# Kernel optimization log

Hardware: AMD Instinct MI355X
Metric: run time of the kernel (lower is better)

## Reference

```python
import jax, jax.numpy as jnp
import numpy as np

N_NODES = 50000
N_EDGES = 1600000
IN_FEAT = 128
OUT_FEAT = 128
NUM_RELS = 40


def setup_inputs() -> dict:
    key = jax.random.key(0)
    ks = jax.random.split(key, 8)
    h = jax.random.normal(ks[0], (N_NODES, IN_FEAT), dtype=jnp.float32)
    # Linear(in_feat, out_feat, bias=False): weight shape [out, in]
    W = jax.random.normal(ks[1], (OUT_FEAT, IN_FEAT), dtype=jnp.float32) / np.sqrt(IN_FEAT)
    # attn_fc: Linear(2*out_feat, 1, bias=False): weight shape [1, 2*out]
    attn_w = jax.random.normal(ks[2], (1, 2 * OUT_FEAT), dtype=jnp.float32) / np.sqrt(2 * OUT_FEAT)
    # Embedding(num_rels, 1, padding_idx=0): row 0 zeroed
    rel_emb = jax.random.normal(ks[3], (NUM_RELS, 1), dtype=jnp.float32)
    rel_emb = rel_emb.at[0].set(0.0)
    stdv = 1.0 / np.sqrt(OUT_FEAT)
    bias_w = jax.random.uniform(ks[4], (OUT_FEAT,), minval=-stdv, maxval=stdv, dtype=jnp.float32)
    src = jax.random.randint(ks[5], (N_EDGES,), 0, N_NODES, dtype=jnp.int32)
    dst = jax.random.randint(ks[6], (N_EDGES,), 0, N_NODES, dtype=jnp.int32)
    etype = jax.random.randint(ks[7], (N_EDGES,), 0, NUM_RELS, dtype=jnp.int32)
    return {"h": h, "W": W, "attn_w": attn_w, "rel_emb": rel_emb,
            "bias_w": bias_w, "src": src, "dst": dst, "etype": etype}


def reference(h, W, attn_w, rel_emb, bias_w, src, dst, etype):
    n = h.shape[0]
    out_feat = W.shape[0]
    # z = weight(h)
    z = h @ W.T  # [N, out]
    # attn_fc(cat(z_src, z_dst)) = z_src @ w1 + z_dst @ w2 (decompose to per-node scores)
    w1 = attn_w[0, :out_feat]
    w2 = attn_w[0, out_feat:]
    s_src = z @ w1  # [N]
    s_dst = z @ w2  # [N]
    e = jax.nn.leaky_relu(s_src[src] + s_dst[dst], negative_slope=0.01)  # [E]
    rel_alpha = rel_emb[etype, 0]  # [E]
    # per-dst-node softmax over incoming edges (ragged mailbox softmax)
    m = jax.ops.segment_max(e, dst, num_segments=n)
    num = jnp.exp(e - m[dst])
    den = jax.ops.segment_sum(num, dst, num_segments=n)
    alpha = num / den[dst]
    # h_dst = sum_e rel_alpha_e * alpha_e * z[src_e]
    w_e = (rel_alpha * alpha)[:, None]  # [E,1]
    h_agg = jax.ops.segment_sum(w_e * z[src], dst, num_segments=n)  # [N, out]
    # RGCNLayer.forward: + bias; no BN/activation for GATLayer; dropout = eval identity
    return h_agg + bias_w
```

## Files before the change

kernel.cpp:

```cpp
#include <hip/hip_runtime.h>
#include <hip/hip_fp16.h>

#define NFEAT 128
#define NBUK_MAX 1024
#define HB 256
#define EPB_MAX 6272
#define BCAP_L 4096
#define HPAD 136

typedef __attribute__((ext_vector_type(8))) _Float16 f16x8;
typedef __attribute__((ext_vector_type(4))) float f32x4;

__global__ __launch_bounds__(256) void k_gemm_mfma(
    const float* __restrict__ h, const float* __restrict__ W,
    const float* __restrict__ attn_w,
    __half* __restrict__ zh, float* __restrict__ s1, float* __restrict__ s2, int n)
{
    __shared__ _Float16 hsh[64 * HPAD];
    __shared__ _Float16 wsh[128 * HPAD];
    const int tid = threadIdx.x;
    const int wv = tid >> 6, lane = tid & 63;
    const int nodeBase = blockIdx.x * 64;

    {
        const float4* W4 = reinterpret_cast<const float4*>(W);
        for (int t = tid; t < 128 * 32; t += 256) {
            int r = t >> 5, c4 = t & 31;
            float4 v = W4[t];
            _Float16* d = &wsh[r * HPAD + c4 * 4];
            d[0] = (_Float16)v.x; d[1] = (_Float16)v.y;
            d[2] = (_Float16)v.z; d[3] = (_Float16)v.w;
        }
    }
    {
        const float4* h4 = reinterpret_cast<const float4*>(h);
        for (int t = tid; t < 64 * 32; t += 256) {
            int r = t >> 5, c4 = t & 31;
            int node = nodeBase + r;
            float4 v = (node < n) ? h4[(size_t)node * 32 + c4]
                                  : make_float4(0.f, 0.f, 0.f, 0.f);
            _Float16* d = &hsh[r * HPAD + c4 * 4];
            d[0] = (_Float16)v.x; d[1] = (_Float16)v.y;
            d[2] = (_Float16)v.z; d[3] = (_Float16)v.w;
        }
    }
    __syncthreads();

    const int arow = lane & 15;
    const int kgrp = lane >> 4;
    f32x4 acc[8];
#pragma unroll
    for (int t = 0; t < 8; ++t) acc[t] = (f32x4){0.f, 0.f, 0.f, 0.f};

#pragma unroll
    for (int k0 = 0; k0 < 128; k0 += 32) {
        f16x8 a = *reinterpret_cast<const f16x8*>(
            &hsh[(wv * 16 + arow) * HPAD + k0 + kgrp * 8]);
#pragma unroll
        for (int nt = 0; nt < 8; ++nt) {
            f16x8 b = *reinterpret_cast<const f16x8*>(
                &wsh[(nt * 16 + arow) * HPAD + k0 + kgrp * 8]);
            acc[nt] = __builtin_amdgcn_mfma_f32_16x16x32_f16(a, b, acc[nt], 0, 0, 0);
        }
    }

    {
        float pr1[4] = {0.f, 0.f, 0.f, 0.f}, pr2[4] = {0.f, 0.f, 0.f, 0.f};
#pragma unroll
        for (int nt = 0; nt < 8; ++nt) {
            float w1v = attn_w[nt * 16 + arow];
            float w2v = attn_w[128 + nt * 16 + arow];
#pragma unroll
            for (int r = 0; r < 4; ++r) {
                pr1[r] += acc[nt][r] * w1v;
                pr2[r] += acc[nt][r] * w2v;
            }
        }
#pragma unroll
        for (int off = 1; off < 16; off <<= 1) {
#pragma unroll
            for (int r = 0; r < 4; ++r) {
                pr1[r] += __shfl_xor(pr1[r], off);
                pr2[r] += __shfl_xor(pr2[r], off);
            }
        }
        if (arow == 0) {
#pragma unroll
            for (int r = 0; r < 4; ++r) {
                int node = nodeBase + wv * 16 + kgrp * 4 + r;
                if (node < n) { s1[node] = pr1[r]; s2[node] = pr2[r]; }
            }
        }
    }

    _Float16* zout = &hsh[wv * 16 * HPAD];
#pragma unroll
    for (int nt = 0; nt < 8; ++nt)
#pragma unroll
        for (int r = 0; r < 4; ++r)
            zout[(kgrp * 4 + r) * HPAD + nt * 16 + arow] = (_Float16)acc[nt][r];

    {
        int node = nodeBase + wv * 16 + arow;
        if (node < n) {
            const uint4* zsrc = reinterpret_cast<const uint4*>(&zout[arow * HPAD + kgrp * 32]);
            uint4* zdst = reinterpret_cast<uint4*>(zh) + (size_t)node * 16 + kgrp * 4;
            uint4 v0 = zsrc[0], v1 = zsrc[1], v2 = zsrc[2], v3 = zsrc[3];
            zdst[0] = v0; zdst[1] = v1; zdst[2] = v2; zdst[3] = v3;
        }
    }
}

__global__ __launch_bounds__(256) void k_hist(const int* __restrict__ dst,
                                              int* __restrict__ hist,
                                              int e, int nbuk, int epb)
{
    __shared__ int lh[NBUK_MAX];
    const int b = blockIdx.x, tid = threadIdx.x;
    for (int k = tid; k < nbuk; k += 256) lh[k] = 0;
    __syncthreads();
    const int beg = b * epb, end = min(e, beg + epb);
    for (int i = beg + tid; i < end; i += 256)
        atomicAdd(&lh[dst[i] >> 6], 1);
    __syncthreads();
    for (int k = tid; k < nbuk; k += 256)
        hist[b * nbuk + k] = lh[k];
}

__global__ __launch_bounds__(256) void k_scan_blocks(const int* __restrict__ hist,
                                                     int* __restrict__ base,
                                                     int* __restrict__ bucket_tot, int nbuk)
{
    __shared__ int wsum[4];
    const int k = blockIdx.x, tid = threadIdx.x;
    int v = hist[tid * nbuk + k];
    int lane = tid & 63, wave = tid >> 6;
    int x = v;
#pragma unroll
    for (int off = 1; off < 64; off <<= 1) {
        int t = __shfl_up(x, off);
        if (lane >= off) x += t;
    }
    if (lane == 63) wsum[wave] = x;
    __syncthreads();
    int wb = 0;
    for (int w = 0; w < wave; ++w) wb += wsum[w];
    base[tid * nbuk + k] = wb + x - v;
    if (tid == 255) bucket_tot[k] = wb + x;
}

__global__ __launch_bounds__(256) void k_scan_buckets(const int* __restrict__ bucket_tot,
                                                      int* __restrict__ bucket_base,
                                                      int* __restrict__ row_start,
                                                      int n, int nbuk)
{
    __shared__ int wsum[4];
    const int tid = threadIdx.x;
    const int C = (nbuk + 255) / 256;
    const int base_i = tid * C;
    int vals[8];
    int s = 0;
#pragma unroll
    for (int j = 0; j < 8; ++j) {
        int v = 0;
        if (j < C) {
            int idx = base_i + j;
            if (idx < nbuk) v = bucket_tot[idx];
        }
        vals[j] = v; s += v;
    }
    int lane = tid & 63, wave = tid >> 6;
    int x = s;
#pragma unroll
    for (int off = 1; off < 64; off <<= 1) {
        int t = __shfl_up(x, off);
        if (lane >= off) x += t;
    }
    if (lane == 63) wsum[wave] = x;
    __syncthreads();
    int wb = 0;
    for (int w = 0; w < wave; ++w) wb += wsum[w];
    int ex = wb + x - s;
#pragma unroll
    for (int j = 0; j < 8; ++j) {
        if (j < C) {
            int idx = base_i + j;
            if (idx < nbuk) bucket_base[idx] = ex;
            ex += vals[j];
        }
    }
    if (tid == 255) row_start[n] = ex;
}

__global__ __launch_bounds__(256) void k_sctr(
    const int* __restrict__ src, const int* __restrict__ dst, const int* __restrict__ etype,
    const int* __restrict__ base, const int* __restrict__ bucket_base,
    unsigned int* __restrict__ bucket_store, int e, int nbuk, int epb)
{
    __shared__ unsigned int est[EPB_MAX];
    __shared__ unsigned short bkt[EPB_MAX];
    __shared__ int lcnt[NBUK_MAX];
    __shared__ int gbase[NBUK_MAX];
    __shared__ int lcur[NBUK_MAX];
    __shared__ int wsum[4];

    const int b = blockIdx.x, tid = threadIdx.x;
    const int beg = b * epb, end = min(e, beg + epb);
    const int cnt = end - beg;

    for (int k = tid; k < nbuk; k += 256) lcnt[k] = 0;
    __syncthreads();
    for (int i = beg + tid; i < end; i += 256)
        atomicAdd(&lcnt[dst[i] >> 6], 1);
    __syncthreads();

    const int C = (nbuk + 255) / 256;
    const int bi = tid * C;
    int vals[4];
    int s = 0;
#pragma unroll
    for (int j = 0; j < 4; ++j) {
        int v = 0;
        if (j < C) {
            int idx = bi + j;
            if (idx < nbuk) v = lcnt[idx];
        }
        vals[j] = v; s += v;
    }
    const int lane = tid & 63, wv = tid >> 6;
    int x = s;
#pragma unroll
    for (int off = 1; off < 64; off <<= 1) {
        int t = __shfl_up(x, off);
        if (lane >= off) x += t;
    }
    if (lane == 63) wsum[wv] = x;
    __syncthreads();
    int wb = 0;
    for (int w = 0; w < wv; ++w) wb += wsum[w];
    int ex = wb + x - s;
#pragma unroll
    for (int j = 0; j < 4; ++j) {
        if (j < C) {
            int idx = bi + j;
            if (idx < nbuk) {
                lcnt[idx] = ex;
                lcur[idx] = ex;
                gbase[idx] = bucket_base[idx] + base[b * nbuk + idx] - ex;
                ex += vals[j];
            }
        }
    }
    __syncthreads();

    for (int i = beg + tid; i < end; i += 256) {
        int d = dst[i];
        int k = d >> 6;
        unsigned int word =
            (unsigned int)src[i] | ((unsigned int)etype[i] << 16) | ((unsigned int)(d & 63) << 22);
        int pos = atomicAdd(&lcur[k], 1);
        est[pos] = word;
        bkt[pos] = (unsigned short)k;
    }
    __syncthreads();

    for (int j = tid; j < cnt; j += 256)
        bucket_store[gbase[bkt[j]] + j] = est[j];
}

__global__ __launch_bounds__(256) void k_place(
    const unsigned int* __restrict__ bucket_store, const int* __restrict__ bucket_tot,
    const int* __restrict__ bucket_base,
    int* __restrict__ row_start, unsigned int* __restrict__ edge_list, int n)
{
    __shared__ unsigned int est[BCAP_L];
    __shared__ int cnt64[64];
    const int b = blockIdx.x;
    const int tid = threadIdx.x;
    const int cnt = min(bucket_tot[b], BCAP_L);
    const int base = bucket_base[b];

    if (tid < 64) cnt64[tid] = 0;
    for (int j = tid; j < cnt; j += 256)
        est[j] = bucket_store[(size_t)base + j];
    __syncthreads();
    for (int j = tid; j < cnt; j += 256)
        atomicAdd(&cnt64[est[j] >> 22], 1);
    __syncthreads();
    if (tid < 64) {
        int v = cnt64[tid];
        int x = v;
#pragma unroll
        for (int off = 1; off < 64; off <<= 1) {
            int t = __shfl_up(x, off);
            if (tid >= off) x += t;
        }
        int node = (b << 6) + tid;
        if (node < n) row_start[node] = base + x - v;
        cnt64[tid] = x - v;
    }
    __syncthreads();
    for (int j = tid; j < cnt; j += 256) {
        unsigned int pk = est[j];
        int pos = base + atomicAdd(&cnt64[pk >> 22], 1);
        edge_list[pos] = pk & 0x3FFFFFu;
    }
}

__global__ __launch_bounds__(256) void k_aggregate(
    const __half* __restrict__ zh, const float* __restrict__ s1, const float* __restrict__ s2,
    const float* __restrict__ rel_emb, const float* __restrict__ bias,
    const int* __restrict__ row_start, const unsigned int* __restrict__ edge_list,
    float* __restrict__ out, int n)
{
    __shared__ uint2 lds_ws[4][64];
    const int wv   = threadIdx.x >> 6;
    const int lane = threadIdx.x & 63;
    const int node = blockIdx.x * 4 + wv;
    if (node >= n) return;

    const int beg = row_start[node];
    const int end = row_start[node + 1];
    const int deg = end - beg;
    const int quad = lane >> 4;
    const int q    = lane & 15;

    float acc[8];
#pragma unroll
    for (int j = 0; j < 8; ++j) acc[j] = 0.f;
    const uint4* z4 = reinterpret_cast<const uint4*>(zh);

    if (deg > 0) {
        const float s2n = s2[node];

        if (deg <= 64) {
            unsigned int pk = 0;
            float ev = -3.4e38f;
            const bool has = lane < deg;
            if (has) {
                pk = edge_list[beg + lane];
                ev = s1[pk & 0xFFFFu] + s2n;
                ev = ev > 0.f ? ev : 0.01f * ev;
            }
            float m = ev;
#pragma unroll
            for (int off = 32; off > 0; off >>= 1)
                m = fmaxf(m, __shfl_xor(m, off));
            float p = has ? __expf(ev - m) : 0.f;
            float den = p;
#pragma unroll
            for (int off = 32; off > 0; off >>= 1)
                den += __shfl_xor(den, off);
            const float inv = 1.f / den;
            const int   src_i = has ? (int)(pk & 0xFFFFu) : 0;
            const float wgt   = has ? rel_emb[pk >> 16] * p * inv : 0.f;

            int jb = 0;
            for (; jb + 16 <= deg; jb += 16) {
                const int j0 = jb + quad;
                int   sA = __shfl(src_i, j0),      sB = __shfl(src_i, j0 + 4);
                int   sC = __shfl(src_i, j0 + 8),  sD = __shfl(src_i, j0 + 12);
                float wA = __shfl(wgt, j0),        wB = __shfl(wgt, j0 + 4);
                float wC = __shfl(wgt, j0 + 8),    wD = __shfl(wgt, j0 + 12);
                uint4 vA = z4[(size_t)sA * 16 + q];
                uint4 vB = z4[(size_t)sB * 16 + q];
                uint4 vC = z4[(size_t)sC * 16 + q];
                uint4 vD = z4[(size_t)sD * 16 + q];
                const __half* hA = reinterpret_cast<const __half*>(&vA);
                const __half* hB = reinterpret_cast<const __half*>(&vB);
                const __half* hC = reinterpret_cast<const __half*>(&vC);
                const __half* hD = reinterpret_cast<const __half*>(&vD);
#pragma unroll
                for (int k2 = 0; k2 < 8; ++k2) {
                    acc[k2] += wA * __half2float(hA[k2]);
                    acc[k2] += wB * __half2float(hB[k2]);
                    acc[k2] += wC * __half2float(hC[k2]);
                    acc[k2] += wD * __half2float(hD[k2]);
                }
            }
            for (; jb < deg; jb += 4) {
                const int j = jb + quad;
                int   sj = __shfl(src_i, j);
                float wj = __shfl(wgt, j);
                uint4 zv = z4[(size_t)sj * 16 + q];
                const __half* hp = reinterpret_cast<const __half*>(&zv);
#pragma unroll
                for (int k2 = 0; k2 < 8; ++k2)
                    acc[k2] += wj * __half2float(hp[k2]);
            }
        } else {
            float mymax = -3.4e38f;
            for (int k = beg + lane; k < end; k += 64) {
                unsigned int pk = edge_list[k];
                float ev = s1[pk & 0xFFFFu] + s2n;
                ev = ev > 0.f ? ev : 0.01f * ev;
                mymax = fmaxf(mymax, ev);
            }
#pragma unroll
            for (int off = 32; off > 0; off >>= 1)
                mymax = fmaxf(mymax, __shfl_xor(mymax, off));
            float mysum = 0.f;
            for (int k = beg + lane; k < end; k += 64) {
                unsigned int pk = edge_list[k];
                float ev = s1[pk & 0xFFFFu] + s2n;
                ev = ev > 0.f ? ev : 0.01f * ev;
                mysum += __expf(ev - mymax);
            }
#pragma unroll
            for (int off = 32; off > 0; off >>= 1)
                mysum += __shfl_xor(mysum, off);
            const float inv = 1.f / mysum;

            for (int cb = beg; cb < end; cb += 64) {
                int k = cb + lane;
                if (k < end) {
                    unsigned int pk = edge_list[k];
                    int s = pk & 0xFFFFu;
                    float ev = s1[s] + s2n;
                    ev = ev > 0.f ? ev : 0.01f * ev;
                    lds_ws[wv][lane] = make_uint2((unsigned)s,
                        __float_as_uint(rel_emb[pk >> 16] * __expf(ev - mymax) * inv));
                }
                int cnt = min(64, end - cb);
#pragma unroll 2
                for (int j = quad; j < cnt; j += 4) {
                    uint2 t = lds_ws[wv][j];
                    float w = __uint_as_float(t.y);
                    uint4 zv = z4[(size_t)t.x * 16 + q];
                    const __half* hp = reinterpret_cast<const __half*>(&zv);
#pragma unroll
                    for (int k2 = 0; k2 < 8; ++k2)
                        acc[k2] += w * __half2float(hp[k2]);
                }
            }
        }
#pragma unroll
        for (int j = 0; j < 8; ++j) {
            acc[j] += __shfl_xor(acc[j], 16);
            acc[j] += __shfl_xor(acc[j], 32);
        }
    }

    if (quad == 0) {
        const float4* b4 = reinterpret_cast<const float4*>(bias);
        float4 b0 = b4[q * 2], b1 = b4[q * 2 + 1];
        float4* o4 = reinterpret_cast<float4*>(out);
        o4[(size_t)node * 32 + q * 2] =
            make_float4(acc[0] + b0.x, acc[1] + b0.y, acc[2] + b0.z, acc[3] + b0.w);
        o4[(size_t)node * 32 + q * 2 + 1] =
            make_float4(acc[4] + b1.x, acc[5] + b1.y, acc[6] + b1.z, acc[7] + b1.w);
    }
}

extern "C" void kernel_launch(void* const* d_in, const int* in_sizes, int n_in,
                              void* d_out, int out_size, void* d_ws, size_t ws_size,
                              hipStream_t stream) {
    const float* h      = (const float*)d_in[0];
    const float* W      = (const float*)d_in[1];
    const float* attn_w = (const float*)d_in[2];
    const float* rel    = (const float*)d_in[3];
    const float* bias   = (const float*)d_in[4];
    const int*   src    = (const int*)d_in[5];
    const int*   dst    = (const int*)d_in[6];
    const int*   etype  = (const int*)d_in[7];
    const int n = in_sizes[0] / NFEAT;
    const int e = in_sizes[5];
    const int nbuk = (n + 63) / 64;
    const int epb = (e + HB - 1) / HB;
    float* out = (float*)d_out;

    char* p = (char*)d_ws;
    __half* zh = (__half*)p;               p += (size_t)n * NFEAT * 2;
    float* s1 = (float*)p;                 p += (size_t)n * 4;
    float* s2 = (float*)p;                 p += (size_t)n * 4;
    int* row_start = (int*)p;              p += (size_t)(n + 1) * 4;
    int* hist       = (int*)p;             p += (size_t)HB * nbuk * 4;
    int* base       = (int*)p;             p += (size_t)HB * nbuk * 4;
    int* bucket_tot = (int*)p;             p += (size_t)nbuk * 4;
    int* bucket_base= (int*)p;             p += (size_t)nbuk * 4;
    unsigned int* edge_list    = (unsigned int*)p;  p += (size_t)e * 4;
    unsigned int* bucket_store = (unsigned int*)p;  p += (size_t)e * 4;

    k_gemm_mfma<<<(n + 63) / 64, 256, 0, stream>>>(h, W, attn_w, zh, s1, s2, n);
    k_hist<<<HB, 256, 0, stream>>>(dst, hist, e, nbuk, epb);
    k_scan_blocks<<<nbuk, 256, 0, stream>>>(hist, base, bucket_tot, nbuk);
    k_scan_buckets<<<1, 256, 0, stream>>>(bucket_tot, bucket_base, row_start, n, nbuk);
    k_sctr<<<HB, 256, 0, stream>>>(src, dst, etype, base, bucket_base, bucket_store, e, nbuk, epb);
    k_place<<<nbuk, 256, 0, stream>>>(bucket_store, bucket_tot, bucket_base, row_start, edge_list, n);
    k_aggregate<<<(n + 3) / 4, 256, 0, stream>>>(zh, s1, s2, rel, bias, row_start, edge_list, out, n);
}
```

Measured before the change: 124.2 us.

## Fold bucket scan into scatter, pre-convert W to fp16, drop LDS staging in place

The single-block bucket-offset scan kernel is removed. Each scatter block now recomputes the bucket prefix sum itself, and block 0 publishes bucket_base, which saves one launch and one serial dependency. W is converted to fp16 once inside the histogram kernel, so each GEMM block copies fp16 rows with 16-byte loads instead of converting the whole weight matrix again. The placement kernel now reads bucket_store twice from global memory instead of staging it in LDS, which removes the 4096-entry capacity cap and writes the row_start bounds per bucket. The trade-off is redundant scan work in every scatter block and extra global reads in the placement kernel.

```diff
diff --git a/kernel.cpp b/kernel.cpp
--- a/kernel.cpp
+++ b/kernel.cpp
@@ -5,14 +5,35 @@
 #define NBUK_MAX 1024
 #define HB 256
 #define EPB_MAX 6272
-#define BCAP_L 4096
 #define HPAD 136
 
 typedef __attribute__((ext_vector_type(8))) _Float16 f16x8;
 typedef __attribute__((ext_vector_type(4))) float f32x4;
 
+__global__ __launch_bounds__(256) void k_hist(const int* __restrict__ dst,
+                                              const float* __restrict__ W,
+                                              _Float16* __restrict__ Wh,
+                                              int* __restrict__ hist,
+                                              int e, int nbuk, int epb)
+{
+    __shared__ int lh[NBUK_MAX];
+    const int b = blockIdx.x, tid = threadIdx.x;
+    if (tid < 64) {
+        int idx = b * 64 + tid;
+        Wh[idx] = (_Float16)W[idx];
+    }
+    for (int k = tid; k < nbuk; k += 256) lh[k] = 0;
+    __syncthreads();
+    const int beg = b * epb, end = min(e, beg + epb);
+    for (int i = beg + tid; i < end; i += 256)
+        atomicAdd(&lh[dst[i] >> 6], 1);
+    __syncthreads();
+    for (int k = tid; k < nbuk; k += 256)
+        hist[b * nbuk + k] = lh[k];
+}
+
 __global__ __launch_bounds__(256) void k_gemm_mfma(
-    const float* __restrict__ h, const float* __restrict__ W,
+    const float* __restrict__ h, const _Float16* __restrict__ Wh,
     const float* __restrict__ attn_w,
     __half* __restrict__ zh, float* __restrict__ s1, float* __restrict__ s2, int n)
 {
@@ -23,13 +44,10 @@
     const int nodeBase = blockIdx.x * 64;
 
     {
-        const float4* W4 = reinterpret_cast<const float4*>(W);
-        for (int t = tid; t < 128 * 32; t += 256) {
-            int r = t >> 5, c4 = t & 31;
-            float4 v = W4[t];
-            _Float16* d = &wsh[r * HPAD + c4 * 4];
-            d[0] = (_Float16)v.x; d[1] = (_Float16)v.y;
-            d[2] = (_Float16)v.z; d[3] = (_Float16)v.w;
+        const uint4* Wv = reinterpret_cast<const uint4*>(Wh);
+        for (int t = tid; t < 2048; t += 256) {
+            int r = t >> 4, c8 = t & 15;
+            *reinterpret_cast<uint4*>(&wsh[r * HPAD + c8 * 8]) = Wv[t];
         }
     }
     {
@@ -111,22 +129,6 @@
     }
 }
 
-__global__ __launch_bounds__(256) void k_hist(const int* __restrict__ dst,
-                                              int* __restrict__ hist,
-                                              int e, int nbuk, int epb)
-{
-    __shared__ int lh[NBUK_MAX];
-    const int b = blockIdx.x, tid = threadIdx.x;
-    for (int k = tid; k < nbuk; k += 256) lh[k] = 0;
-    __syncthreads();
-    const int beg = b * epb, end = min(e, beg + epb);
-    for (int i = beg + tid; i < end; i += 256)
-        atomicAdd(&lh[dst[i] >> 6], 1);
-    __syncthreads();
-    for (int k = tid; k < nbuk; k += 256)
-        hist[b * nbuk + k] = lh[k];
-}
-
 __global__ __launch_bounds__(256) void k_scan_blocks(const int* __restrict__ hist,
                                                      int* __restrict__ base,
                                                      int* __restrict__ bucket_tot, int nbuk)
@@ -149,52 +151,10 @@
     if (tid == 255) bucket_tot[k] = wb + x;
 }
 
-__global__ __launch_bounds__(256) void k_scan_buckets(const int* __restrict__ bucket_tot,
-                                                      int* __restrict__ bucket_base,
-                                                      int* __restrict__ row_start,
-                                                      int n, int nbuk)
-{
-    __shared__ int wsum[4];
-    const int tid = threadIdx.x;
-    const int C = (nbuk + 255) / 256;
-    const int base_i = tid * C;
-    int vals[8];
-    int s = 0;
-#pragma unroll
-    for (int j = 0; j < 8; ++j) {
-        int v = 0;
-        if (j < C) {
-            int idx = base_i + j;
-            if (idx < nbuk) v = bucket_tot[idx];
-        }
-        vals[j] = v; s += v;
-    }
-    int lane = tid & 63, wave = tid >> 6;
-    int x = s;
-#pragma unroll
-    for (int off = 1; off < 64; off <<= 1) {
-        int t = __shfl_up(x, off);
-        if (lane >= off) x += t;
-    }
-    if (lane == 63) wsum[wave] = x;
-    __syncthreads();
-    int wb = 0;
-    for (int w = 0; w < wave; ++w) wb += wsum[w];
-    int ex = wb + x - s;
-#pragma unroll
-    for (int j = 0; j < 8; ++j) {
-        if (j < C) {
-            int idx = base_i + j;
-            if (idx < nbuk) bucket_base[idx] = ex;
-            ex += vals[j];
-        }
-    }
-    if (tid == 255) row_start[n] = ex;
-}
-
 __global__ __launch_bounds__(256) void k_sctr(
     const int* __restrict__ src, const int* __restrict__ dst, const int* __restrict__ etype,
-    const int* __restrict__ base, const int* __restrict__ bucket_base,
+    const int* __restrict__ base, const int* __restrict__ bucket_tot,
+    int* __restrict__ bucket_base,
     unsigned int* __restrict__ bucket_store, int e, int nbuk, int epb)
 {
     __shared__ unsigned int est[EPB_MAX];
@@ -207,47 +167,85 @@
     const int b = blockIdx.x, tid = threadIdx.x;
     const int beg = b * epb, end = min(e, beg + epb);
     const int cnt = end - beg;
+    const int lane = tid & 63, wv = tid >> 6;
+    const int C = (nbuk + 255) / 256;
+    const int bi = tid * C;
 
     for (int k = tid; k < nbuk; k += 256) lcnt[k] = 0;
-    __syncthreads();
+
+    {
+        int vals[4];
+        int s = 0;
+#pragma unroll
+        for (int j = 0; j < 4; ++j) {
+            int v = 0;
+            if (j < C) {
+                int idx = bi + j;
+                if (idx < nbuk) v = bucket_tot[idx];
+            }
+            vals[j] = v; s += v;
+        }
+        int x = s;
+#pragma unroll
+        for (int off = 1; off < 64; off <<= 1) {
+            int t = __shfl_up(x, off);
+            if (lane >= off) x += t;
+        }
+        if (lane == 63) wsum[wv] = x;
+        __syncthreads();
+        int wb = 0;
+        for (int w = 0; w < wv; ++w) wb += wsum[w];
+        int ex = wb + x - s;
+#pragma unroll
+        for (int j = 0; j < 4; ++j) {
+            if (j < C) {
+                int idx = bi + j;
+                if (idx < nbuk) {
+                    gbase[idx] = ex;
+                    if (b == 0) bucket_base[idx] = ex;
+                    ex += vals[j];
+                }
+            }
+        }
+    }
+    __syncthreads();
+
     for (int i = beg + tid; i < end; i += 256)
         atomicAdd(&lcnt[dst[i] >> 6], 1);
     __syncthreads();
 
-    const int C = (nbuk + 255) / 256;
-    const int bi = tid * C;
-    int vals[4];
-    int s = 0;
-#pragma unroll
-    for (int j = 0; j < 4; ++j) {
-        int v = 0;
-        if (j < C) {
-            int idx = bi + j;
-            if (idx < nbuk) v = lcnt[idx];
-        }
-        vals[j] = v; s += v;
-    }
-    const int lane = tid & 63, wv = tid >> 6;
-    int x = s;
-#pragma unroll
-    for (int off = 1; off < 64; off <<= 1) {
-        int t = __shfl_up(x, off);
-        if (lane >= off) x += t;
-    }
-    if (lane == 63) wsum[wv] = x;
-    __syncthreads();
-    int wb = 0;
-    for (int w = 0; w < wv; ++w) wb += wsum[w];
-    int ex = wb + x - s;
-#pragma unroll
-    for (int j = 0; j < 4; ++j) {
-        if (j < C) {
-            int idx = bi + j;
-            if (idx < nbuk) {
-                lcnt[idx] = ex;
-                lcur[idx] = ex;
-                gbase[idx] = bucket_base[idx] + base[b * nbuk + idx] - ex;
-                ex += vals[j];
+    {
+        int vals[4];
+        int s = 0;
+#pragma unroll
+        for (int j = 0; j < 4; ++j) {
+            int v = 0;
+            if (j < C) {
+                int idx = bi + j;
+                if (idx < nbuk) v = lcnt[idx];
+            }
+            vals[j] = v; s += v;
+        }
+        int x = s;
+#pragma unroll
+        for (int off = 1; off < 64; off <<= 1) {
+            int t = __shfl_up(x, off);
+            if (lane >= off) x += t;
+        }
+        if (lane == 63) wsum[wv] = x;
+        __syncthreads();
+        int wb = 0;
+        for (int w = 0; w < wv; ++w) wb += wsum[w];
+        int ex = wb + x - s;
+#pragma unroll
+        for (int j = 0; j < 4; ++j) {
+            if (j < C) {
+                int idx = bi + j;
+                if (idx < nbuk) {
+                    lcur[idx] = ex;
+                    gbase[idx] = gbase[idx] + base[b * nbuk + idx] - ex;
+                    ex += vals[j];
+                }
             }
         }
     }
@@ -273,19 +271,16 @@
     const int* __restrict__ bucket_base,
     int* __restrict__ row_start, unsigned int* __restrict__ edge_list, int n)
 {
-    __shared__ unsigned int est[BCAP_L];
     __shared__ int cnt64[64];
     const int b = blockIdx.x;
     const int tid = threadIdx.x;
-    const int cnt = min(bucket_tot[b], BCAP_L);
+    const int cnt = bucket_tot[b];
     const int base = bucket_base[b];
 
     if (tid < 64) cnt64[tid] = 0;
+    __syncthreads();
     for (int j = tid; j < cnt; j += 256)
-        est[j] = bucket_store[(size_t)base + j];
-    __syncthreads();
-    for (int j = tid; j < cnt; j += 256)
-        atomicAdd(&cnt64[est[j] >> 22], 1);
+        atomicAdd(&cnt64[bucket_store[(size_t)base + j] >> 22], 1);
     __syncthreads();
     if (tid < 64) {
         int v = cnt64[tid];
@@ -299,9 +294,14 @@
         if (node < n) row_start[node] = base + x - v;
         cnt64[tid] = x - v;
     }
+    if (tid == 0) {
+        int bnd = (b << 6) + 64;
+        if (bnd > n) bnd = n;
+        row_start[bnd] = base + cnt;
+    }
     __syncthreads();
     for (int j = tid; j < cnt; j += 256) {
-        unsigned int pk = est[j];
+        unsigned int pk = bucket_store[(size_t)base + j];
         int pos = base + atomicAdd(&cnt64[pk >> 22], 1);
         edge_list[pos] = pk & 0x3FFFFFu;
     }
@@ -473,6 +473,7 @@
     __half* zh = (__half*)p;               p += (size_t)n * NFEAT * 2;
     float* s1 = (float*)p;                 p += (size_t)n * 4;
     float* s2 = (float*)p;                 p += (size_t)n * 4;
+    _Float16* Wh = (_Float16*)p;           p += (size_t)NFEAT * NFEAT * 2;
     int* row_start = (int*)p;              p += (size_t)(n + 1) * 4;
     int* hist       = (int*)p;             p += (size_t)HB * nbuk * 4;
     int* base       = (int*)p;             p += (size_t)HB * nbuk * 4;
@@ -481,11 +482,12 @@
     unsigned int* edge_list    = (unsigned int*)p;  p += (size_t)e * 4;
     unsigned int* bucket_store = (unsigned int*)p;  p += (size_t)e * 4;
 
-    k_gemm_mfma<<<(n + 63) / 64, 256, 0, stream>>>(h, W, attn_w, zh, s1, s2, n);
-    k_hist<<<HB, 256, 0, stream>>>(dst, hist, e, nbuk, epb);
+    k_hist<<<HB, 256, 0, stream>>>(dst, W, Wh, hist, e, nbuk, epb);
+    k_gemm_mfma<<<(n + 63) / 64, 256, 0, stream>>>(h, Wh, attn_w, zh, s1, s2, n);
     k_scan_blocks<<<nbuk, 256, 0, stream>>>(hist, base, bucket_tot, nbuk);
-    k_scan_buckets<<<1, 256, 0, stream>>>(bucket_tot, bucket_base, row_start, n, nbuk);
-    k_sctr<<<HB, 256, 0, stream>>>(src, dst, etype, base, bucket_base, bucket_store, e, nbuk, epb);
-    k_place<<<nbuk, 256, 0, stream>>>(bucket_store, bucket_tot, bucket_base, row_start, edge_list, n);
+    k_sctr<<<HB, 256, 0, stream>>>(src, dst, etype, base, bucket_tot, bucket_base,
+                                   bucket_store, e, nbuk, epb);
+    k_place<<<nbuk, 256, 0, stream>>>(bucket_store, bucket_tot, bucket_base,
+                                      row_start, edge_list, n);
     k_aggregate<<<(n + 3) / 4, 256, 0, stream>>>(zh, s1, s2, rel, bias, row_start, edge_list, out, n);
 }
```

After: 120.9 us. -2.7%, faster.
